# Kernel tuning notes

Measured on AMD Instinct MI355X. Metric: run time of the kernel, lower is better.

The kernel has to match this reference:

```python
import jax, jax.numpy as jnp
import numpy as np

N_NODES = 60000
N_EDGES = 120000
N_GRAPHS = 2048
ATOM_DIM = 4
H = 192            # hidden_dim
NL = 5             # n_layers
ND = 200           # n_descriptors
EDGE_DIM = 1


def setup_inputs() -> dict:
    key = jax.random.key(0)
    ks = jax.random.split(key, 16)

    def w(k, shape, fan_in):
        return jax.random.normal(k, shape, jnp.float32) * (1.0 / np.sqrt(fan_in))

    M_IN = 2 * H + EDGE_DIM  # message MLP input: [x_src, x_dst, edge_attr]
    M_H = 2 * H              # MPNNLayer(hidden_dim=hidden_dim*2)
    inp = {
        "atom_features": jax.random.normal(ks[0], (N_NODES, ATOM_DIM), jnp.float32),
        "edge_attr": jax.random.normal(ks[1], (N_EDGES, EDGE_DIM), jnp.float32),
        "edge_index": jax.random.randint(ks[2], (2, N_EDGES), 0, N_NODES),
        "batch": jnp.sort(jax.random.randint(ks[3], (N_NODES,), 0, N_GRAPHS)),
        # atom encoder: Linear + GELU + LayerNorm
        "enc_w": w(ks[4], (ATOM_DIM, H), ATOM_DIM), "enc_b": jnp.zeros((H,), jnp.float32),
        "enc_ln_g": jnp.ones((H,), jnp.float32), "enc_ln_b": jnp.zeros((H,), jnp.float32),
        # 5 MPNN layers (stacked params)
        "msg_w1": w(ks[5], (NL, M_IN, M_H), M_IN), "msg_b1": jnp.zeros((NL, M_H), jnp.float32),
        "msg_w2": w(ks[6], (NL, M_H, H), M_H), "msg_b2": jnp.zeros((NL, H), jnp.float32),
        "upd_w": w(ks[7], (NL, 2 * H, H), 2 * H), "upd_b": jnp.zeros((NL, H), jnp.float32),
        "ln_g": jnp.ones((NL, H), jnp.float32), "ln_b": jnp.zeros((NL, H), jnp.float32),
        # head MLP: 2H -> H -> H//2 -> ND
        "h1_w": w(ks[8], (2 * H, H), 2 * H), "h1_b": jnp.zeros((H,), jnp.float32),
        "h2_w": w(ks[9], (H, H // 2), H), "h2_b": jnp.zeros((H // 2,), jnp.float32),
        "h3_w": w(ks[10], (H // 2, ND), H // 2), "h3_b": jnp.zeros((ND,), jnp.float32),
    }
    return inp


def _ln(x, g, b, eps=1e-5):
    mu = x.mean(-1, keepdims=True)
    v = x.var(-1, keepdims=True)
    return (x - mu) / jnp.sqrt(v + eps) * g + b


def _gelu(x):
    return jax.nn.gelu(x, approximate=False)  # torch nn.GELU (erf)


def _forward(atom_features, edge_attr, enc_w, enc_b, enc_ln_g, enc_ln_b,
             msg_w1, msg_b1, msg_w2, msg_b2, upd_w, upd_b, ln_g, ln_b,
             h1_w, h1_b, h2_w, h2_b, h3_w, h3_b, edge_index, batch):
    src, dst = edge_index[0], edge_index[1]
    x = _ln(_gelu(atom_features @ enc_w + enc_b), enc_ln_g, enc_ln_b)  # [N, H]
    for l in range(NL):
        # gather endpoints -> message MLP -> scatter-sum to dst
        m_in = jnp.concatenate([x[src], x[dst], edge_attr], axis=-1)   # [E, 2H+1]
        m = _gelu(m_in @ msg_w1[l] + msg_b1[l]) @ msg_w2[l] + msg_b2[l]  # [E, H]
        agg = jax.ops.segment_sum(m, dst, num_segments=N_NODES)        # [N, H]
        x_new = _gelu(jnp.concatenate([x, agg], axis=-1) @ upd_w[l] + upd_b[l])
        x = _ln(x + x_new, ln_g[l], ln_b[l])  # residual + LN (dropout = eval identity)
    # per-graph mean/max pooling (segment reductions)
    cnt = jax.ops.segment_sum(jnp.ones((x.shape[0],), x.dtype), batch, num_segments=N_GRAPHS)
    s = jax.ops.segment_sum(x, batch, num_segments=N_GRAPHS)
    mean_pool = jnp.where(cnt[:, None] > 0, s / jnp.maximum(cnt, 1.0)[:, None], 0.0)
    max_pool = jax.ops.segment_max(x, batch, num_segments=N_GRAPHS)  # -inf for empty, as torch
    g = jnp.concatenate([mean_pool, max_pool], axis=-1)  # [G, 2H]
    h = _gelu(g @ h1_w + h1_b)
    h = _gelu(h @ h2_w + h2_b)
    return h @ h3_w + h3_b  # [G, ND]


def reference(atom_features, edge_attr, edge_index, batch, enc_w, enc_b, enc_ln_g, enc_ln_b,
              msg_w1, msg_b1, msg_w2, msg_b2, upd_w, upd_b, ln_g, ln_b,
              h1_w, h1_b, h2_w, h2_b, h3_w, h3_b):
    return _forward(atom_features, edge_attr, enc_w, enc_b, enc_ln_g, enc_ln_b,
                    msg_w1, msg_b1, msg_w2, msg_b2, upd_w, upd_b, ln_g, ln_b,
                    h1_w, h1_b, h2_w, h2_b, h3_w, h3_b, edge_index, batch)
```

## Files before the change

### kernel.cpp

```cpp
#include <hip/hip_runtime.h>

#define H 192
#define NL 5
#define NN 60000
#define NE 120000
#define NG 2048
#define ND 200
#define LDA 392
#define NT 128
#define LDU 200

typedef __bf16 bfrag __attribute__((ext_vector_type(8)));
typedef __bf16 bf16x4 __attribute__((ext_vector_type(4)));
typedef float f32x4 __attribute__((ext_vector_type(4)));

__device__ __forceinline__ unsigned short f2bf(float f) {
  union { float f; unsigned u; } v; v.f = f;
  return (unsigned short)((v.u + 0x7FFFu + ((v.u >> 16) & 1u)) >> 16);
}
__device__ __forceinline__ float bflo(unsigned u) {
  union { unsigned u; float f; } v; v.u = u << 16; return v.f;
}
__device__ __forceinline__ float bfhi(unsigned u) {
  union { unsigned u; float f; } v; v.u = u & 0xffff0000u; return v.f;
}
__device__ __forceinline__ float gelu(float x) {
  const float t = exp2f(x * (-2.3020922f - 0.10293942f * x * x));
  return x * __frcp_rn(1.f + t);
}

__global__ __launch_bounds__(256) void prep_kernel(
    const float* __restrict__ msg_w1, const float* __restrict__ msg_w2,
    const float* __restrict__ upd_w, const float* __restrict__ h1_w,
    const float* __restrict__ h2_w, const float* __restrict__ h3_w,
    unsigned short* __restrict__ W1f, float* __restrict__ w1last,
    unsigned short* __restrict__ W2f, unsigned short* __restrict__ Uf,
    unsigned short* __restrict__ h1f, unsigned short* __restrict__ h2f,
    unsigned short* __restrict__ h3f) {
  int idx = blockIdx.x * 256 + threadIdx.x;
  const int SW1 = NL * 147456;
  const int S2 = NL * 384;
  const int SW2 = NL * 73728;
  if (idx < SW1) {
    int l = idx / 147456, r = idx % 147456;
    int i = r & 7, lane = (r >> 3) & 63, t = r >> 9;
    int kk = t % 12, jblk = t / 12;
    int j = jblk * 16 + (lane & 15);
    int k = kk * 32 + ((lane >> 4) << 3) + i;
    W1f[idx] = f2bf(msg_w1[(size_t)l * 385 * 384 + (size_t)k * 384 + j]);
    return;
  }
  idx -= SW1;
  if (idx < S2) {
    int l = idx / 384, j = idx % 384;
    w1last[idx] = msg_w1[(size_t)l * 385 * 384 + 384 * 384 + j];
    return;
  }
  idx -= S2;
  if (idx < SW2) {
    int l = idx / 73728, r = idx % 73728;
    int i = r & 7, lane = (r >> 3) & 63, t = r >> 9;
    int kk = t % 12, jblk = t / 12;
    int j = jblk * 16 + (lane & 15);
    int k = kk * 32 + ((lane >> 4) << 3) + i;
    W2f[idx] = f2bf(msg_w2[(size_t)l * 384 * 192 + (size_t)k * 192 + j]);
    return;
  }
  idx -= SW2;
  if (idx < SW2) {
    int l = idx / 73728, r = idx % 73728;
    int i = r & 7, lane = (r >> 3) & 63, t = r >> 9;
    int kk = t % 12, jblk = t / 12;
    int j = jblk * 16 + (lane & 15);
    int k = kk * 32 + ((lane >> 4) << 3) + i;
    Uf[idx] = f2bf(upd_w[(size_t)l * 384 * 192 + (size_t)k * 192 + j]);
    return;
  }
  idx -= SW2;
  if (idx < 73728) {
    int i = idx & 7, lane = (idx >> 3) & 63, t = idx >> 9;
    int kk = t % 12, jblk = t / 12;
    int j = jblk * 16 + (lane & 15);
    int k = kk * 32 + ((lane >> 4) << 3) + i;
    h1f[idx] = f2bf(h1_w[(size_t)k * 192 + j]);
    return;
  }
  idx -= 73728;
  if (idx < 18432) {
    int i = idx & 7, lane = (idx >> 3) & 63, t = idx >> 9;
    int kk = t % 6, jblk = t / 6;
    int j = jblk * 16 + (lane & 15);
    int k = kk * 32 + ((lane >> 4) << 3) + i;
    h2f[idx] = f2bf(h2_w[(size_t)k * 96 + j]);
    return;
  }
  idx -= 18432;
  if (idx < 19968) {
    int i = idx & 7, lane = (idx >> 3) & 63, t = idx >> 9;
    int kk = t % 3, jblk = t / 3;
    int j = jblk * 16 + (lane & 15);
    int k = kk * 32 + ((lane >> 4) << 3) + i;
    h3f[idx] = (j < 200) ? f2bf(h3_w[(size_t)k * 200 + j]) : (unsigned short)0;
    return;
  }
}

__global__ __launch_bounds__(256) void enc_kernel(
    const float* __restrict__ af, const float* __restrict__ w,
    const float* __restrict__ b, const float* __restrict__ g,
    const float* __restrict__ bb, float* __restrict__ x,
    __bf16* __restrict__ xb) {
  const int node = blockIdx.x * 4 + (threadIdx.x >> 6);
  const int lane = threadIdx.x & 63;
  if (node >= NN) return;
  const float a0 = af[node * 4 + 0], a1 = af[node * 4 + 1];
  const float a2 = af[node * 4 + 2], a3 = af[node * 4 + 3];
  float v[3], s = 0.f, ss = 0.f;
#pragma unroll
  for (int i = 0; i < 3; ++i) {
    const int j = lane + i * 64;
    float o = a0 * w[j] + a1 * w[H + j] + a2 * w[2 * H + j] + a3 * w[3 * H + j] + b[j];
    o = gelu(o);
    v[i] = o; s += o; ss += o * o;
  }
#pragma unroll
  for (int m = 1; m < 64; m <<= 1) { s += __shfl_xor(s, m); ss += __shfl_xor(ss, m); }
  const float mu = s * (1.f / H);
  float var = ss * (1.f / H) - mu * mu;
  const float rstd = rsqrtf(fmaxf(var, 0.f) + 1e-5f);
#pragma unroll
  for (int i = 0; i < 3; ++i) {
    const int j = lane + i * 64;
    const float o = (v[i] - mu) * rstd * g[j] + bb[j];
    x[(size_t)node * H + j] = o;
    xb[(size_t)node * H + j] = (__bf16)o;
  }
}

__global__ __launch_bounds__(256) void csr_count(const int* __restrict__ ei,
                                                 int* __restrict__ deg) {
  const int e = blockIdx.x * 256 + threadIdx.x;
  if (e < NE) atomicAdd(&deg[ei[NE + e]], 1);
}

__global__ __launch_bounds__(1024) void csr_scan(const int* __restrict__ deg,
                                                 int* __restrict__ start) {
  __shared__ int wsum[16];
  const int tid = threadIdx.x, lane = tid & 63, wv = tid >> 6;
  int carry = 0;
  for (int base = 0; base < NN; base += 1024) {
    const int i = base + tid;
    int v = (i < NN) ? deg[i] : 0;
    int s = v;
#pragma unroll
    for (int d = 1; d < 64; d <<= 1) {
      int t = __shfl_up(s, d);
      if (lane >= d) s += t;
    }
    if (lane == 63) wsum[wv] = s;
    __syncthreads();
    if (wv == 0) {
      int ws_ = (lane < 16) ? wsum[lane] : 0;
#pragma unroll
      for (int d = 1; d < 16; d <<= 1) {
        int t = __shfl_up(ws_, d);
        if (lane >= d) ws_ += t;
      }
      if (lane < 16) wsum[lane] = ws_;
    }
    __syncthreads();
    const int woff = (wv == 0) ? 0 : wsum[wv - 1];
    if (i < NN) start[i] = carry + woff + s - v;
    carry += wsum[15];
    __syncthreads();
  }
  if (tid == 0) start[NN] = NE;
}

__global__ __launch_bounds__(256) void csr_fill(const int* __restrict__ ei,
                                                const int* __restrict__ start,
                                                int* __restrict__ cur,
                                                int* __restrict__ eidx) {
  const int e = blockIdx.x * 256 + threadIdx.x;
  if (e < NE) {
    const int d = ei[NE + e];
    const int p = start[d] + atomicAdd(&cur[d], 1);
    eidx[p] = e;
  }
}

__global__ __launch_bounds__(256) void gseg_kernel(const int* __restrict__ batch,
                                                   int* __restrict__ gstart,
                                                   int* __restrict__ gend) {
  const int i = blockIdx.x * 256 + threadIdx.x;
  if (i >= NN) return;
  const int b = batch[i];
  if (i == 0 || batch[i - 1] != b) gstart[b] = i;
  if (i == NN - 1 || batch[i + 1] != b) gend[b] = i + 1;
}

__global__ __launch_bounds__(512, 4) void msg_kernel(
    const __bf16* __restrict__ xb, const int* __restrict__ ei,
    const float* __restrict__ ea, const unsigned short* __restrict__ W1f,
    const float* __restrict__ w1last, const float* __restrict__ b1,
    const unsigned short* __restrict__ W2f, const float* __restrict__ b2,
    unsigned short* __restrict__ m) {
  __shared__ unsigned short A[64 * LDA];
  __shared__ float eaS[64];
  const int tid = threadIdx.x;
  const int wave = tid >> 6, lane = tid & 63;
  const int lrow = lane & 15, kgrp = lane >> 4;
  const int tile = blockIdx.x * 64;

  if (tid < 64) eaS[tid] = ea[tile + tid];
  {
    const int r = tid >> 3, s = tid & 7;
    const int e = tile + r;
    const uint4* ps = (const uint4*)(xb + (size_t)ei[e] * H);
    const uint4* pd = (const uint4*)(xb + (size_t)ei[NE + e] * H);
#pragma unroll
    for (int i = 0; i < 3; ++i)
      *(uint4*)(&A[r * LDA + (s + 8 * i) * 8]) = ps[s + 8 * i];
#pragma unroll
    for (int i = 3; i < 6; ++i)
      *(uint4*)(&A[r * LDA + (s + 8 * i) * 8]) = pd[s + 8 * i - 24];
  }
  __syncthreads();

  const int jb16 = wave * 3;
  f32x4 acc[3][4];
#pragma unroll
  for (int mf = 0; mf < 3; ++mf)
#pragma unroll
    for (int eb = 0; eb < 4; ++eb)
#pragma unroll
      for (int q = 0; q < 4; ++q) acc[mf][eb][q] = 0.f;

#pragma unroll 2
  for (int kk = 0; kk < 12; ++kk) {
    const int k0 = kk * 32 + kgrp * 8;
    bfrag bF[4];
#pragma unroll
    for (int eb = 0; eb < 4; ++eb)
      bF[eb] = *(const bfrag*)(&A[(eb * 16 + lrow) * LDA + k0]);
#pragma unroll
    for (int mf = 0; mf < 3; ++mf) {
      const bfrag aF = *(const bfrag*)(W1f + ((size_t)((jb16 + mf) * 12 + kk) * 64 + lane) * 8);
#pragma unroll
      for (int eb = 0; eb < 4; ++eb)
        acc[mf][eb] = __builtin_amdgcn_mfma_f32_16x16x32_bf16(aF, bF[eb], acc[mf][eb], 0, 0, 0);
    }
  }
  __syncthreads();

#pragma unroll
  for (int mf = 0; mf < 3; ++mf) {
    const int j0 = (jb16 + mf) * 16 + kgrp * 4;
    const float bi0 = b1[j0], bi1 = b1[j0 + 1], bi2 = b1[j0 + 2], bi3 = b1[j0 + 3];
    const float wl0 = w1last[j0], wl1 = w1last[j0 + 1], wl2 = w1last[j0 + 2], wl3 = w1last[j0 + 3];
#pragma unroll
    for (int eb = 0; eb < 4; ++eb) {
      const int e = eb * 16 + lrow;
      const float eav = eaS[e];
      bf16x4 v;
      v[0] = (__bf16)gelu(acc[mf][eb][0] + bi0 + eav * wl0);
      v[1] = (__bf16)gelu(acc[mf][eb][1] + bi1 + eav * wl1);
      v[2] = (__bf16)gelu(acc[mf][eb][2] + bi2 + eav * wl2);
      v[3] = (__bf16)gelu(acc[mf][eb][3] + bi3 + eav * wl3);
      *(bf16x4*)(&A[e * LDA + j0]) = v;
    }
  }
  __syncthreads();

  const int jcnt2 = (wave < 4) ? 2 : 1;
  const int j2b0 = (wave < 4) ? (wave * 2) : (4 + wave);
  f32x4 acc2[2][4];
#pragma unroll
  for (int a = 0; a < 2; ++a)
#pragma unroll
    for (int eb = 0; eb < 4; ++eb)
#pragma unroll
      for (int q = 0; q < 4; ++q) acc2[a][eb][q] = 0.f;

#pragma unroll 2
  for (int kk = 0; kk < 12; ++kk) {
    const int k0 = kk * 32 + kgrp * 8;
    bfrag bF[4];
#pragma unroll
    for (int eb = 0; eb < 4; ++eb)
      bF[eb] = *(const bfrag*)(&A[(eb * 16 + lrow) * LDA + k0]);
#pragma unroll
    for (int a = 0; a < 2; ++a) {
      if (a < jcnt2) {
        const bfrag aF = *(const bfrag*)(W2f + ((size_t)((j2b0 + a) * 12 + kk) * 64 + lane) * 8);
#pragma unroll
        for (int eb = 0; eb < 4; ++eb)
          acc2[a][eb] = __builtin_amdgcn_mfma_f32_16x16x32_bf16(aF, bF[eb], acc2[a][eb], 0, 0, 0);
      }
    }
  }
#pragma unroll
  for (int a = 0; a < 2; ++a) {
    if (a < jcnt2) {
      const int j0 = (j2b0 + a) * 16 + kgrp * 4;
      const float bi0 = b2[j0], bi1 = b2[j0 + 1], bi2 = b2[j0 + 2], bi3 = b2[j0 + 3];
#pragma unroll
      for (int eb = 0; eb < 4; ++eb) {
        const int e = eb * 16 + lrow;
        bf16x4 v;
        v[0] = (__bf16)(acc2[a][eb][0] + bi0);
        v[1] = (__bf16)(acc2[a][eb][1] + bi1);
        v[2] = (__bf16)(acc2[a][eb][2] + bi2);
        v[3] = (__bf16)(acc2[a][eb][3] + bi3);
        *(bf16x4*)(m + (size_t)(tile + e) * H + j0) = v;
      }
    }
  }
}

__global__ __launch_bounds__(512, 4) void upd_kernel(
    const unsigned short* __restrict__ Uf, const float* __restrict__ ub,
    const float* __restrict__ lng, const float* __restrict__ lnb,
    const unsigned short* __restrict__ m, const int* __restrict__ start,
    const int* __restrict__ eidx, float* x, __bf16* xb) {
  __shared__ unsigned short A[NT * LDU];
  __shared__ float wsm[8][NT];
  __shared__ float wsq[8][NT];
  __shared__ float mur[NT], rsr[NT];
  const int tid = threadIdx.x;
  const int wave = tid >> 6, lane = tid & 63;
  const int lrow = lane & 15, kgrp = lane >> 4;
  const int tile = blockIdx.x * NT;

  const int r = tid >> 2, q4 = tid & 3;
  const int node = tile + r;
  if (node < NN) {
    const uint4* px = (const uint4*)(xb + (size_t)node * H + q4 * 48);
#pragma unroll
    for (int i = 0; i < 6; ++i)
      *(uint4*)(&A[r * LDU + q4 * 48 + i * 8]) = px[i];
  } else {
#pragma unroll
    for (int i = 0; i < 6; ++i)
      *(uint4*)(&A[r * LDU + q4 * 48 + i * 8]) = make_uint4(0, 0, 0, 0);
  }
  __syncthreads();

  const int jcnt = (wave < 4) ? 2 : 1;
  const int jb0 = (wave < 4) ? (wave * 2) : (4 + wave);

  f32x4 acc[2][8];
#pragma unroll
  for (int a = 0; a < 2; ++a)
#pragma unroll
    for (int eb = 0; eb < 8; ++eb)
#pragma unroll
      for (int q = 0; q < 4; ++q) acc[a][eb][q] = 0.f;

#pragma unroll 1
  for (int kk = 0; kk < 6; ++kk) {
    const int k0 = kk * 32 + kgrp * 8;
    bfrag bF[8];
#pragma unroll
    for (int eb = 0; eb < 8; ++eb)
      bF[eb] = *(const bfrag*)(&A[(eb * 16 + lrow) * LDU + k0]);
#pragma unroll
    for (int a = 0; a < 2; ++a) {
      if (a < jcnt) {
        const bfrag aF = *(const bfrag*)(Uf + ((size_t)((jb0 + a) * 12 + kk) * 64 + lane) * 8);
#pragma unroll
        for (int eb = 0; eb < 8; ++eb)
          acc[a][eb] = __builtin_amdgcn_mfma_f32_16x16x32_bf16(aF, bF[eb], acc[a][eb], 0, 0, 0);
      }
    }
  }
  __syncthreads();

  if (node < NN) {
    const int p0 = start[node], p1 = start[node + 1];
#pragma unroll
    for (int hh = 0; hh < 2; ++hh) {
      const int c0 = q4 * 48 + hh * 24;
      float av[24];
#pragma unroll
      for (int i = 0; i < 24; ++i) av[i] = 0.f;
      for (int p = p0; p < p1; ++p) {
        const int e = eidx[p];
        const uint4* mr = (const uint4*)(m + (size_t)e * H + c0);
#pragma unroll
        for (int i = 0; i < 3; ++i) {
          const uint4 u = mr[i];
          av[i * 8 + 0] += bflo(u.x); av[i * 8 + 1] += bfhi(u.x);
          av[i * 8 + 2] += bflo(u.y); av[i * 8 + 3] += bfhi(u.y);
          av[i * 8 + 4] += bflo(u.z); av[i * 8 + 5] += bfhi(u.z);
          av[i * 8 + 6] += bflo(u.w); av[i * 8 + 7] += bfhi(u.w);
        }
      }
#pragma unroll
      for (int i = 0; i < 24; i += 4) {
        bf16x4 v;
        v[0] = (__bf16)av[i]; v[1] = (__bf16)av[i + 1];
        v[2] = (__bf16)av[i + 2]; v[3] = (__bf16)av[i + 3];
        *(bf16x4*)(&A[r * LDU + c0 + i]) = v;
      }
    }
  } else {
#pragma unroll
    for (int i = 0; i < 48; i += 8)
      *(uint4*)(&A[r * LDU + q4 * 48 + i]) = make_uint4(0, 0, 0, 0);
  }
  __syncthreads();

#pragma unroll 1
  for (int kk = 0; kk < 6; ++kk) {
    const int k0 = kk * 32 + kgrp * 8;
    bfrag bF[8];
#pragma unroll
    for (int eb = 0; eb < 8; ++eb)
      bF[eb] = *(const bfrag*)(&A[(eb * 16 + lrow) * LDU + k0]);
#pragma unroll
    for (int a = 0; a < 2; ++a) {
      if (a < jcnt) {
        const bfrag aF = *(const bfrag*)(Uf + ((size_t)((jb0 + a) * 12 + 6 + kk) * 64 + lane) * 8);
#pragma unroll
        for (int eb = 0; eb < 8; ++eb)
          acc[a][eb] = __builtin_amdgcn_mfma_f32_16x16x32_bf16(aF, bF[eb], acc[a][eb], 0, 0, 0);
      }
    }
  }

  float lsum[8], lsq[8];
#pragma unroll
  for (int eb = 0; eb < 8; ++eb) { lsum[eb] = 0.f; lsq[eb] = 0.f; }
#pragma unroll
  for (int a = 0; a < 2; ++a) {
    if (a < jcnt) {
      const int jb = (jb0 + a) * 16 + kgrp * 4;
      const float4 ub4 = *(const float4*)(ub + jb);
#pragma unroll
      for (int eb = 0; eb < 8; ++eb) {
        const int n2 = tile + eb * 16 + lrow;
        if (n2 < NN) {
          const float4 xr = *(const float4*)(x + (size_t)n2 * H + jb);
          acc[a][eb][0] = xr.x + gelu(acc[a][eb][0] + ub4.x);
          acc[a][eb][1] = xr.y + gelu(acc[a][eb][1] + ub4.y);
          acc[a][eb][2] = xr.z + gelu(acc[a][eb][2] + ub4.z);
          acc[a][eb][3] = xr.w + gelu(acc[a][eb][3] + ub4.w);
        } else {
          acc[a][eb][0] = 0.f; acc[a][eb][1] = 0.f;
          acc[a][eb][2] = 0.f; acc[a][eb][3] = 0.f;
        }
#pragma unroll
        for (int q = 0; q < 4; ++q) {
          lsum[eb] += acc[a][eb][q];
          lsq[eb] += acc[a][eb][q] * acc[a][eb][q];
        }
      }
    }
  }
#pragma unroll
  for (int eb = 0; eb < 8; ++eb) {
    lsum[eb] += __shfl_xor(lsum[eb], 16);
    lsum[eb] += __shfl_xor(lsum[eb], 32);
    lsq[eb] += __shfl_xor(lsq[eb], 16);
    lsq[eb] += __shfl_xor(lsq[eb], 32);
  }
  if (kgrp == 0) {
#pragma unroll
    for (int eb = 0; eb < 8; ++eb) {
      wsm[wave][eb * 16 + lrow] = lsum[eb];
      wsq[wave][eb * 16 + lrow] = lsq[eb];
    }
  }
  __syncthreads();
  if (tid < NT) {
    float s = 0.f, sq = 0.f;
#pragma unroll
    for (int w2 = 0; w2 < 8; ++w2) { s += wsm[w2][tid]; sq += wsq[w2][tid]; }
    const float mu = s * (1.f / H);
    float var = sq * (1.f / H) - mu * mu;
    mur[tid] = mu;
    rsr[tid] = rsqrtf(fmaxf(var, 0.f) + 1e-5f);
  }
  __syncthreads();
#pragma unroll
  for (int a = 0; a < 2; ++a) {
    if (a < jcnt) {
      const int jb = (jb0 + a) * 16 + kgrp * 4;
      const float4 g4 = *(const float4*)(lng + jb);
      const float4 b4 = *(const float4*)(lnb + jb);
#pragma unroll
      for (int eb = 0; eb < 8; ++eb) {
        const int nc = eb * 16 + lrow;
        const int n2 = tile + nc;
        if (n2 < NN) {
          const float mu = mur[nc], rs = rsr[nc];
          float4 o;
          o.x = (acc[a][eb][0] - mu) * rs * g4.x + b4.x;
          o.y = (acc[a][eb][1] - mu) * rs * g4.y + b4.y;
          o.z = (acc[a][eb][2] - mu) * rs * g4.z + b4.z;
          o.w = (acc[a][eb][3] - mu) * rs * g4.w + b4.w;
          *(float4*)(x + (size_t)n2 * H + jb) = o;
          bf16x4 ob;
          ob[0] = (__bf16)o.x; ob[1] = (__bf16)o.y;
          ob[2] = (__bf16)o.z; ob[3] = (__bf16)o.w;
          *(bf16x4*)(xb + (size_t)n2 * H + jb) = ob;
        }
      }
    }
  }
}

__global__ __launch_bounds__(256) void pool_kernel(
    const float* __restrict__ x, const int* __restrict__ gstart,
    const int* __restrict__ gend, __bf16* __restrict__ Gb) {
  const int w = threadIdx.x >> 6, lane = threadIdx.x & 63;
  const int gi = blockIdx.x * 4 + w;
  const int n0 = gstart[gi], n1 = gend[gi];
  float sm[3] = {0.f, 0.f, 0.f};
  float mx[3] = {-INFINITY, -INFINITY, -INFINITY};
  for (int n = n0; n < n1; ++n) {
#pragma unroll
    for (int i = 0; i < 3; ++i) {
      const float v = x[(size_t)n * H + lane + i * 64];
      sm[i] += v; mx[i] = fmaxf(mx[i], v);
    }
  }
  const int cnt = n1 - n0;
  const float inv = cnt > 0 ? 1.f / (float)cnt : 0.f;
#pragma unroll
  for (int i = 0; i < 3; ++i) {
    const int j = lane + i * 64;
    Gb[(size_t)gi * 384 + j] = (__bf16)(sm[i] * inv);
    Gb[(size_t)gi * 384 + 192 + j] = (__bf16)mx[i];
  }
}

__global__ __launch_bounds__(512) void head_kernel(
    const __bf16* __restrict__ Gb,
    const unsigned short* __restrict__ h1f, const float* __restrict__ h1b,
    const unsigned short* __restrict__ h2f, const float* __restrict__ h2b,
    const unsigned short* __restrict__ h3f, const float* __restrict__ h3b,
    float* __restrict__ out) {
  __shared__ unsigned short A[32 * LDA];
  const int tid = threadIdx.x;
  const int wave = tid >> 6, lane = tid & 63;
  const int lrow = lane & 15, kgrp = lane >> 4;
  const int tile = blockIdx.x * 32;

  {
    const int r = tid >> 4, s = tid & 15;
    const uint4* pg = (const uint4*)(Gb + (size_t)(tile + r) * 384);
#pragma unroll
    for (int i = 0; i < 3; ++i)
      *(uint4*)(&A[r * LDA + (s + 16 * i) * 8]) = pg[s + 16 * i];
  }
  __syncthreads();

  const int jcnt1 = (wave < 4) ? 2 : 1;
  const int jb1 = (wave < 4) ? (wave * 2) : (4 + wave);
  f32x4 acc[2][2];
#pragma unroll
  for (int a = 0; a < 2; ++a)
#pragma unroll
    for (int eb = 0; eb < 2; ++eb)
#pragma unroll
      for (int q = 0; q < 4; ++q) acc[a][eb][q] = 0.f;
#pragma unroll 2
  for (int kk = 0; kk < 12; ++kk) {
    const int k0 = kk * 32 + kgrp * 8;
    bfrag bF[2];
#pragma unroll
    for (int eb = 0; eb < 2; ++eb)
      bF[eb] = *(const bfrag*)(&A[(eb * 16 + lrow) * LDA + k0]);
#pragma unroll
    for (int a = 0; a < 2; ++a) {
      if (a < jcnt1) {
        const bfrag aF = *(const bfrag*)(h1f + ((size_t)((jb1 + a) * 12 + kk) * 64 + lane) * 8);
#pragma unroll
        for (int eb = 0; eb < 2; ++eb)
          acc[a][eb] = __builtin_amdgcn_mfma_f32_16x16x32_bf16(aF, bF[eb], acc[a][eb], 0, 0, 0);
      }
    }
  }
  __syncthreads();
#pragma unroll
  for (int a = 0; a < 2; ++a) {
    if (a < jcnt1) {
      const int j0 = (jb1 + a) * 16 + kgrp * 4;
      const float4 b4 = *(const float4*)(h1b + j0);
#pragma unroll
      for (int eb = 0; eb < 2; ++eb) {
        const int g = eb * 16 + lrow;
        bf16x4 v;
        v[0] = (__bf16)gelu(acc[a][eb][0] + b4.x);
        v[1] = (__bf16)gelu(acc[a][eb][1] + b4.y);
        v[2] = (__bf16)gelu(acc[a][eb][2] + b4.z);
        v[3] = (__bf16)gelu(acc[a][eb][3] + b4.w);
        *(bf16x4*)(&A[g * LDA + j0]) = v;
      }
    }
  }
  __syncthreads();

  f32x4 acc2[2];
#pragma unroll
  for (int eb = 0; eb < 2; ++eb)
#pragma unroll
    for (int q = 0; q < 4; ++q) acc2[eb][q] = 0.f;
  if (wave < 6) {
#pragma unroll 2
    for (int kk = 0; kk < 6; ++kk) {
      const int k0 = kk * 32 + kgrp * 8;
      bfrag bF[2];
#pragma unroll
      for (int eb = 0; eb < 2; ++eb)
        bF[eb] = *(const bfrag*)(&A[(eb * 16 + lrow) * LDA + k0]);
      const bfrag aF = *(const bfrag*)(h2f + ((size_t)(wave * 6 + kk) * 64 + lane) * 8);
#pragma unroll
      for (int eb = 0; eb < 2; ++eb)
        acc2[eb] = __builtin_amdgcn_mfma_f32_16x16x32_bf16(aF, bF[eb], acc2[eb], 0, 0, 0);
    }
    const int j0 = wave * 16 + kgrp * 4;
    const float4 b4 = *(const float4*)(h2b + j0);
#pragma unroll
    for (int eb = 0; eb < 2; ++eb) {
      const int g = eb * 16 + lrow;
      bf16x4 v;
      v[0] = (__bf16)gelu(acc2[eb][0] + b4.x);
      v[1] = (__bf16)gelu(acc2[eb][1] + b4.y);
      v[2] = (__bf16)gelu(acc2[eb][2] + b4.z);
      v[3] = (__bf16)gelu(acc2[eb][3] + b4.w);
      *(bf16x4*)(&A[g * LDA + 192 + j0]) = v;
    }
  }
  __syncthreads();

  const int jcnt3 = (wave < 5) ? 2 : 1;
  const int jb3 = (wave < 5) ? (wave * 2) : (wave + 5);
  f32x4 acc3[2][2];
#pragma unroll
  for (int a = 0; a < 2; ++a)
#pragma unroll
    for (int eb = 0; eb < 2; ++eb)
#pragma unroll
      for (int q = 0; q < 4; ++q) acc3[a][eb][q] = 0.f;
#pragma unroll
  for (int kk = 0; kk < 3; ++kk) {
    const int k0 = 192 + kk * 32 + kgrp * 8;
    bfrag bF[2];
#pragma unroll
    for (int eb = 0; eb < 2; ++eb)
      bF[eb] = *(const bfrag*)(&A[(eb * 16 + lrow) * LDA + k0]);
#pragma unroll
    for (int a = 0; a < 2; ++a) {
      if (a < jcnt3) {
        const bfrag aF = *(const bfrag*)(h3f + ((size_t)((jb3 + a) * 3 + kk) * 64 + lane) * 8);
#pragma unroll
        for (int eb = 0; eb < 2; ++eb)
          acc3[a][eb] = __builtin_amdgcn_mfma_f32_16x16x32_bf16(aF, bF[eb], acc3[a][eb], 0, 0, 0);
      }
    }
  }
#pragma unroll
  for (int a = 0; a < 2; ++a) {
    if (a < jcnt3) {
      const int jb = jb3 + a;
      const int j0 = jb * 16 + kgrp * 4;
#pragma unroll
      for (int eb = 0; eb < 2; ++eb) {
        const int g = tile + eb * 16 + lrow;
        if (jb < 12) {
          const float4 b4 = *(const float4*)(h3b + j0);
          float4 o;
          o.x = acc3[a][eb][0] + b4.x;
          o.y = acc3[a][eb][1] + b4.y;
          o.z = acc3[a][eb][2] + b4.z;
          o.w = acc3[a][eb][3] + b4.w;
          *(float4*)(out + (size_t)g * ND + j0) = o;
        } else {
#pragma unroll
          for (int t = 0; t < 4; ++t) {
            const int j = j0 + t;
            if (j < ND) out[(size_t)g * ND + j] = acc3[a][eb][t] + h3b[j];
          }
        }
      }
    }
  }
}

extern "C" void kernel_launch(void* const* d_in, const int* in_sizes, int n_in,
                              void* d_out, int out_size, void* d_ws, size_t ws_size,
                              hipStream_t stream) {
  const float* atom   = (const float*)d_in[0];
  const float* ea     = (const float*)d_in[1];
  const int*   ei     = (const int*)d_in[2];
  const int*   batch  = (const int*)d_in[3];
  const float* enc_w  = (const float*)d_in[4];
  const float* enc_b  = (const float*)d_in[5];
  const float* enc_lng= (const float*)d_in[6];
  const float* enc_lnb= (const float*)d_in[7];
  const float* msg_w1 = (const float*)d_in[8];
  const float* msg_b1 = (const float*)d_in[9];
  const float* msg_w2 = (const float*)d_in[10];
  const float* msg_b2 = (const float*)d_in[11];
  const float* upd_w  = (const float*)d_in[12];
  const float* upd_b  = (const float*)d_in[13];
  const float* ln_g   = (const float*)d_in[14];
  const float* ln_b   = (const float*)d_in[15];
  const float* h1_w   = (const float*)d_in[16];
  const float* h1_b   = (const float*)d_in[17];
  const float* h2_w   = (const float*)d_in[18];
  const float* h2_b   = (const float*)d_in[19];
  const float* h3_w   = (const float*)d_in[20];
  const float* h3_b   = (const float*)d_in[21];
  float* out = (float*)d_out;

  char* ws = (char*)d_ws;
  size_t off = 0;
  auto alloc = [&](size_t bytes) -> void* {
    void* p = ws + off;
    off = (off + bytes + 255) & ~(size_t)255;
    return p;
  };
  float* x            = (float*)alloc((size_t)NN * H * 4);
  __bf16* xb          = (__bf16*)alloc((size_t)NN * H * 2);
  unsigned short* msg = (unsigned short*)alloc((size_t)NE * H * 2);
  unsigned short* W1f = (unsigned short*)alloc((size_t)NL * 147456 * 2);
  float* w1last       = (float*)alloc((size_t)NL * 384 * 4);
  unsigned short* W2f = (unsigned short*)alloc((size_t)NL * 73728 * 2);
  unsigned short* Uf  = (unsigned short*)alloc((size_t)NL * 73728 * 2);
  unsigned short* h1f = (unsigned short*)alloc((size_t)73728 * 2);
  unsigned short* h2f = (unsigned short*)alloc((size_t)18432 * 2);
  unsigned short* h3f = (unsigned short*)alloc((size_t)19968 * 2);
  __bf16* Gb          = (__bf16*)alloc((size_t)NG * 384 * 2);
  int* deg            = (int*)alloc((size_t)NN * 4);
  int* cstart         = (int*)alloc((size_t)(NN + 1) * 4);
  int* eidx           = (int*)alloc((size_t)NE * 4);
  int* gstart         = (int*)alloc((size_t)NG * 4);
  int* gend           = (int*)alloc((size_t)NG * 4);

  prep_kernel<<<6206, 256, 0, stream>>>(msg_w1, msg_w2, upd_w, h1_w, h2_w, h3_w,
                                        W1f, w1last, W2f, Uf, h1f, h2f, h3f);
  enc_kernel<<<NN / 4, 256, 0, stream>>>(atom, enc_w, enc_b, enc_lng, enc_lnb, x, xb);

  hipMemsetAsync(deg, 0, (size_t)NN * 4, stream);
  csr_count<<<(NE + 255) / 256, 256, 0, stream>>>(ei, deg);
  csr_scan<<<1, 1024, 0, stream>>>(deg, cstart);
  hipMemsetAsync(deg, 0, (size_t)NN * 4, stream);
  csr_fill<<<(NE + 255) / 256, 256, 0, stream>>>(ei, cstart, deg, eidx);

  hipMemsetAsync(gstart, 0, (size_t)NG * 4, stream);
  hipMemsetAsync(gend, 0, (size_t)NG * 4, stream);
  gseg_kernel<<<(NN + 255) / 256, 256, 0, stream>>>(batch, gstart, gend);

  for (int l = 0; l < NL; ++l) {
    msg_kernel<<<NE / 64, 512, 0, stream>>>(
        xb, ei, ea, W1f + (size_t)l * 147456, w1last + l * 384,
        msg_b1 + l * 384, W2f + (size_t)l * 73728, msg_b2 + l * 192, msg);
    upd_kernel<<<(NN + NT - 1) / NT, 512, 0, stream>>>(
        Uf + (size_t)l * 73728, upd_b + l * 192, ln_g + l * 192,
        ln_b + l * 192, msg, cstart, eidx, x, xb);
  }
  pool_kernel<<<NG / 4, 256, 0, stream>>>(x, gstart, gend, Gb);
  head_kernel<<<NG / 32, 512, 0, stream>>>(Gb, h1f, h1_b, h2f, h2_b, h3f, h3_b, out);
}
```

Measured before the change: 853.6 us.

## Fold message second linear into update weights, drop agg GEMM in update

Precomputes W2·U_agg and b2·U_agg per layer on device, so the message kernel emits messages already projected through the update's aggregate half. The update kernel then adds the summed projected messages plus degree times the folded bias directly, skipping the second 192-wide K half of its GEMM. Pooling now reads bf16 xb instead of fp32 x, and the head kernel gains an extra barrier. This saves update GEMM work and pooling bandwidth, at the cost of an extra fold kernel and bf16 rounding of folded weights and pooled inputs.

New measurement: 850.9 us. About the same (-0.3%).

```diff
diff --git a/kernel.cpp b/kernel.cpp
--- a/kernel.cpp
+++ b/kernel.cpp
@@ -29,18 +29,58 @@
   return x * __frcp_rn(1.f + t);
 }
 
+__global__ __launch_bounds__(256) void fold_kernel(
+    const float* __restrict__ msg_w2, const float* __restrict__ upd_w,
+    const float* __restrict__ msg_b2, float* __restrict__ W2p,
+    float* __restrict__ v2) {
+  __shared__ float row4[4][192];
+  const int bid = blockIdx.x;
+  const int l = bid / 97, sub = bid % 97;
+  const int j = threadIdx.x;
+  const int nr = (sub < 96) ? 4 : 1;
+  if (j < 192) {
+    if (sub < 96) {
+      const int k0 = sub * 4;
+#pragma unroll
+      for (int rr = 0; rr < 4; ++rr)
+        row4[rr][j] = msg_w2[(size_t)l * 384 * 192 + (size_t)(k0 + rr) * 192 + j];
+    } else {
+      row4[0][j] = msg_b2[l * 192 + j];
+    }
+  }
+  __syncthreads();
+  if (j >= 192) return;
+  const float* Ua = upd_w + (size_t)l * 384 * 192 + (size_t)192 * 192;
+  float acc[4] = {0.f, 0.f, 0.f, 0.f};
+  for (int t = 0; t < 192; ++t) {
+    const float u = Ua[t * 192 + j];
+#pragma unroll
+    for (int rr = 0; rr < 4; ++rr) acc[rr] += row4[rr][t] * u;
+  }
+  if (sub < 96) {
+    const int k0 = sub * 4;
+#pragma unroll
+    for (int rr = 0; rr < 4; ++rr)
+      W2p[(size_t)l * 384 * 192 + (size_t)(k0 + rr) * 192 + j] = acc[rr];
+  } else {
+    v2[l * 192 + j] = acc[0];
+  }
+  (void)nr;
+}
+
 __global__ __launch_bounds__(256) void prep_kernel(
-    const float* __restrict__ msg_w1, const float* __restrict__ msg_w2,
+    const float* __restrict__ msg_w1, const float* __restrict__ W2p,
     const float* __restrict__ upd_w, const float* __restrict__ h1_w,
     const float* __restrict__ h2_w, const float* __restrict__ h3_w,
     unsigned short* __restrict__ W1f, float* __restrict__ w1last,
-    unsigned short* __restrict__ W2f, unsigned short* __restrict__ Uf,
+    unsigned short* __restrict__ W2f, unsigned short* __restrict__ Uxf,
     unsigned short* __restrict__ h1f, unsigned short* __restrict__ h2f,
     unsigned short* __restrict__ h3f) {
   int idx = blockIdx.x * 256 + threadIdx.x;
   const int SW1 = NL * 147456;
   const int S2 = NL * 384;
   const int SW2 = NL * 73728;
+  const int SUX = NL * 36864;
   if (idx < SW1) {
     int l = idx / 147456, r = idx % 147456;
     int i = r & 7, lane = (r >> 3) & 63, t = r >> 9;
@@ -63,20 +103,20 @@
     int kk = t % 12, jblk = t / 12;
     int j = jblk * 16 + (lane & 15);
     int k = kk * 32 + ((lane >> 4) << 3) + i;
-    W2f[idx] = f2bf(msg_w2[(size_t)l * 384 * 192 + (size_t)k * 192 + j]);
+    W2f[idx] = f2bf(W2p[(size_t)l * 384 * 192 + (size_t)k * 192 + j]);
     return;
   }
   idx -= SW2;
-  if (idx < SW2) {
-    int l = idx / 73728, r = idx % 73728;
+  if (idx < SUX) {
+    int l = idx / 36864, r = idx % 36864;
     int i = r & 7, lane = (r >> 3) & 63, t = r >> 9;
-    int kk = t % 12, jblk = t / 12;
+    int kk = t % 6, jblk = t / 6;
     int j = jblk * 16 + (lane & 15);
     int k = kk * 32 + ((lane >> 4) << 3) + i;
-    Uf[idx] = f2bf(upd_w[(size_t)l * 384 * 192 + (size_t)k * 192 + j]);
+    Uxf[idx] = f2bf(upd_w[(size_t)l * 384 * 192 + (size_t)k * 192 + j]);
     return;
   }
-  idx -= SW2;
+  idx -= SUX;
   if (idx < 73728) {
     int i = idx & 7, lane = (idx >> 3) & 63, t = idx >> 9;
     int kk = t % 12, jblk = t / 12;
@@ -203,8 +243,7 @@
     const __bf16* __restrict__ xb, const int* __restrict__ ei,
     const float* __restrict__ ea, const unsigned short* __restrict__ W1f,
     const float* __restrict__ w1last, const float* __restrict__ b1,
-    const unsigned short* __restrict__ W2f, const float* __restrict__ b2,
-    unsigned short* __restrict__ m) {
+    const unsigned short* __restrict__ W2f, unsigned short* __restrict__ m) {
   __shared__ unsigned short A[64 * LDA];
   __shared__ float eaS[64];
   const int tid = threadIdx.x;
@@ -303,15 +342,14 @@
   for (int a = 0; a < 2; ++a) {
     if (a < jcnt2) {
       const int j0 = (j2b0 + a) * 16 + kgrp * 4;
-      const float bi0 = b2[j0], bi1 = b2[j0 + 1], bi2 = b2[j0 + 2], bi3 = b2[j0 + 3];
 #pragma unroll
       for (int eb = 0; eb < 4; ++eb) {
         const int e = eb * 16 + lrow;
         bf16x4 v;
-        v[0] = (__bf16)(acc2[a][eb][0] + bi0);
-        v[1] = (__bf16)(acc2[a][eb][1] + bi1);
-        v[2] = (__bf16)(acc2[a][eb][2] + bi2);
-        v[3] = (__bf16)(acc2[a][eb][3] + bi3);
+        v[0] = (__bf16)acc2[a][eb][0];
+        v[1] = (__bf16)acc2[a][eb][1];
+        v[2] = (__bf16)acc2[a][eb][2];
+        v[3] = (__bf16)acc2[a][eb][3];
         *(bf16x4*)(m + (size_t)(tile + e) * H + j0) = v;
       }
     }
@@ -319,14 +357,16 @@
 }
 
 __global__ __launch_bounds__(512, 4) void upd_kernel(
-    const unsigned short* __restrict__ Uf, const float* __restrict__ ub,
-    const float* __restrict__ lng, const float* __restrict__ lnb,
-    const unsigned short* __restrict__ m, const int* __restrict__ start,
-    const int* __restrict__ eidx, float* x, __bf16* xb) {
+    const unsigned short* __restrict__ Uxf, const float* __restrict__ ub,
+    const float* __restrict__ v2, const float* __restrict__ lng,
+    const float* __restrict__ lnb, const unsigned short* __restrict__ m,
+    const int* __restrict__ start, const int* __restrict__ eidx,
+    float* x, __bf16* xb) {
   __shared__ unsigned short A[NT * LDU];
   __shared__ float wsm[8][NT];
   __shared__ float wsq[8][NT];
   __shared__ float mur[NT], rsr[NT];
+  __shared__ float degS[NT];
   const int tid = threadIdx.x;
   const int wave = tid >> 6, lane = tid & 63;
   const int lrow = lane & 15, kgrp = lane >> 4;
@@ -367,7 +407,7 @@
 #pragma unroll
     for (int a = 0; a < 2; ++a) {
       if (a < jcnt) {
-        const bfrag aF = *(const bfrag*)(Uf + ((size_t)((jb0 + a) * 12 + kk) * 64 + lane) * 8);
+        const bfrag aF = *(const bfrag*)(Uxf + ((size_t)((jb0 + a) * 6 + kk) * 64 + lane) * 8);
 #pragma unroll
         for (int eb = 0; eb < 8; ++eb)
           acc[a][eb] = __builtin_amdgcn_mfma_f32_16x16x32_bf16(aF, bF[eb], acc[a][eb], 0, 0, 0);
@@ -378,6 +418,7 @@
 
   if (node < NN) {
     const int p0 = start[node], p1 = start[node + 1];
+    if (q4 == 0) degS[r] = (float)(p1 - p0);
 #pragma unroll
     for (int hh = 0; hh < 2; ++hh) {
       const int c0 = q4 * 48 + hh * 24;
@@ -405,29 +446,12 @@
       }
     }
   } else {
+    if (q4 == 0) degS[r] = 0.f;
 #pragma unroll
     for (int i = 0; i < 48; i += 8)
       *(uint4*)(&A[r * LDU + q4 * 48 + i]) = make_uint4(0, 0, 0, 0);
   }
   __syncthreads();
-
-#pragma unroll 1
-  for (int kk = 0; kk < 6; ++kk) {
-    const int k0 = kk * 32 + kgrp * 8;
-    bfrag bF[8];
-#pragma unroll
-    for (int eb = 0; eb < 8; ++eb)
-      bF[eb] = *(const bfrag*)(&A[(eb * 16 + lrow) * LDU + k0]);
-#pragma unroll
-    for (int a = 0; a < 2; ++a) {
-      if (a < jcnt) {
-        const bfrag aF = *(const bfrag*)(Uf + ((size_t)((jb0 + a) * 12 + 6 + kk) * 64 + lane) * 8);
-#pragma unroll
-        for (int eb = 0; eb < 8; ++eb)
-          acc[a][eb] = __builtin_amdgcn_mfma_f32_16x16x32_bf16(aF, bF[eb], acc[a][eb], 0, 0, 0);
-      }
-    }
-  }
 
   float lsum[8], lsq[8];
 #pragma unroll
@@ -437,15 +461,19 @@
     if (a < jcnt) {
       const int jb = (jb0 + a) * 16 + kgrp * 4;
       const float4 ub4 = *(const float4*)(ub + jb);
+      const float4 v24 = *(const float4*)(v2 + jb);
 #pragma unroll
       for (int eb = 0; eb < 8; ++eb) {
-        const int n2 = tile + eb * 16 + lrow;
+        const int nc = eb * 16 + lrow;
+        const int n2 = tile + nc;
         if (n2 < NN) {
+          const bf16x4 ag = *(const bf16x4*)(&A[nc * LDU + jb]);
+          const float d = degS[nc];
           const float4 xr = *(const float4*)(x + (size_t)n2 * H + jb);
-          acc[a][eb][0] = xr.x + gelu(acc[a][eb][0] + ub4.x);
-          acc[a][eb][1] = xr.y + gelu(acc[a][eb][1] + ub4.y);
-          acc[a][eb][2] = xr.z + gelu(acc[a][eb][2] + ub4.z);
-          acc[a][eb][3] = xr.w + gelu(acc[a][eb][3] + ub4.w);
+          acc[a][eb][0] = xr.x + gelu(acc[a][eb][0] + (float)ag[0] + d * v24.x + ub4.x);
+          acc[a][eb][1] = xr.y + gelu(acc[a][eb][1] + (float)ag[1] + d * v24.y + ub4.y);
+          acc[a][eb][2] = xr.z + gelu(acc[a][eb][2] + (float)ag[2] + d * v24.z + ub4.z);
+          acc[a][eb][3] = xr.w + gelu(acc[a][eb][3] + (float)ag[3] + d * v24.w + ub4.w);
         } else {
           acc[a][eb][0] = 0.f; acc[a][eb][1] = 0.f;
           acc[a][eb][2] = 0.f; acc[a][eb][3] = 0.f;
@@ -512,7 +540,7 @@
 }
 
 __global__ __launch_bounds__(256) void pool_kernel(
-    const float* __restrict__ x, const int* __restrict__ gstart,
+    const __bf16* __restrict__ xb, const int* __restrict__ gstart,
     const int* __restrict__ gend, __bf16* __restrict__ Gb) {
   const int w = threadIdx.x >> 6, lane = threadIdx.x & 63;
   const int gi = blockIdx.x * 4 + w;
@@ -522,7 +550,7 @@
   for (int n = n0; n < n1; ++n) {
 #pragma unroll
     for (int i = 0; i < 3; ++i) {
-      const float v = x[(size_t)n * H + lane + i * 64];
+      const float v = (float)xb[(size_t)n * H + lane + i * 64];
       sm[i] += v; mx[i] = fmaxf(mx[i], v);
     }
   }
@@ -621,6 +649,9 @@
       for (int eb = 0; eb < 2; ++eb)
         acc2[eb] = __builtin_amdgcn_mfma_f32_16x16x32_bf16(aF, bF[eb], acc2[eb], 0, 0, 0);
     }
+  }
+  __syncthreads();
+  if (wave < 6) {
     const int j0 = wave * 16 + kgrp * 4;
     const float4 b4 = *(const float4*)(h2b + j0);
 #pragma unroll
@@ -730,7 +761,9 @@
   unsigned short* W1f = (unsigned short*)alloc((size_t)NL * 147456 * 2);
   float* w1last       = (float*)alloc((size_t)NL * 384 * 4);
   unsigned short* W2f = (unsigned short*)alloc((size_t)NL * 73728 * 2);
-  unsigned short* Uf  = (unsigned short*)alloc((size_t)NL * 73728 * 2);
+  unsigned short* Uxf = (unsigned short*)alloc((size_t)NL * 36864 * 2);
+  float* W2p          = (float*)alloc((size_t)NL * 384 * 192 * 4);
+  float* v2           = (float*)alloc((size_t)NL * 192 * 4);
   unsigned short* h1f = (unsigned short*)alloc((size_t)73728 * 2);
   unsigned short* h2f = (unsigned short*)alloc((size_t)18432 * 2);
   unsigned short* h3f = (unsigned short*)alloc((size_t)19968 * 2);
@@ -741,8 +774,9 @@
   int* gstart         = (int*)alloc((size_t)NG * 4);
   int* gend           = (int*)alloc((size_t)NG * 4);
 
-  prep_kernel<<<6206, 256, 0, stream>>>(msg_w1, msg_w2, upd_w, h1_w, h2_w, h3_w,
-                                        W1f, w1last, W2f, Uf, h1f, h2f, h3f);
+  fold_kernel<<<NL * 97, 256, 0, stream>>>(msg_w2, upd_w, msg_b2, W2p, v2);
+  prep_kernel<<<5486, 256, 0, stream>>>(msg_w1, W2p, upd_w, h1_w, h2_w, h3_w,
+                                        W1f, w1last, W2f, Uxf, h1f, h2f, h3f);
   enc_kernel<<<NN / 4, 256, 0, stream>>>(atom, enc_w, enc_b, enc_lng, enc_lnb, x, xb);
 
   hipMemsetAsync(deg, 0, (size_t)NN * 4, stream);
@@ -758,11 +792,11 @@
   for (int l = 0; l < NL; ++l) {
     msg_kernel<<<NE / 64, 512, 0, stream>>>(
         xb, ei, ea, W1f + (size_t)l * 147456, w1last + l * 384,
-        msg_b1 + l * 384, W2f + (size_t)l * 73728, msg_b2 + l * 192, msg);
+        msg_b1 + l * 384, W2f + (size_t)l * 73728, msg);
     upd_kernel<<<(NN + NT - 1) / NT, 512, 0, stream>>>(
-        Uf + (size_t)l * 73728, upd_b + l * 192, ln_g + l * 192,
-        ln_b + l * 192, msg, cstart, eidx, x, xb);
-  }
-  pool_kernel<<<NG / 4, 256, 0, stream>>>(x, gstart, gend, Gb);
+        Uxf + (size_t)l * 36864, upd_b + l * 192, v2 + l * 192,
+        ln_g + l * 192, ln_b + l * 192, msg, cstart, eidx, x, xb);
+  }
+  pool_kernel<<<NG / 4, 256, 0, stream>>>(xb, gstart, gend, Gb);
   head_kernel<<<NG / 32, 512, 0, stream>>>(Gb, h1f, h1_b, h2f, h2_b, h3f, h3_b, out);
 }
```
